# Performance work log

Measured on AMD Instinct MI355X. Metric: run time of the kernel, lower is better.

The kernel has to match this reference:

```python
import jax, jax.numpy as jnp
import numpy as np

E = 8      # num_experts
D = 1024   # input_size
H = 1024   # hidden_size
K = 2      # top_k
B = 2
S = 1024


def setup_inputs() -> dict:
    key = jax.random.key(0)
    ks = jax.random.split(key, 5)
    x = jax.random.normal(ks[0], (B, S, D), dtype=jnp.float32)
    p = jax.random.uniform(ks[1], (B * S, K), dtype=jnp.float32)
    expert_p = p / p.sum(axis=-1, keepdims=True)            # normalized top-k gates
    expert_idxs = jax.random.randint(ks[2], (B * S, K), 0, E)
    W1 = jax.random.normal(ks[3], (E, D, 2 * H), dtype=jnp.float32) * (D ** -0.5)
    W2 = jax.random.normal(ks[4], (E, H, D), dtype=jnp.float32) * (H ** -0.5)
    return {"x": x, "expert_p": expert_p, "expert_idxs": expert_idxs, "W1": W1, "W2": W2}


def reference(x, expert_p, expert_idxs, W1, W2):
    x_shape = x.shape
    xf = x.reshape(-1, x_shape[-1])                 # [N, D]
    n_tok = xf.shape[0]
    k = expert_idxs.shape[-1]
    x_pair = jnp.repeat(xf, k, axis=0)              # [N*K, D] token replicated per expert slot
    idx = expert_idxs.reshape(-1)                   # [N*K]
    p = expert_p.reshape(-1)                        # [N*K]
    y_pair = jnp.zeros((n_tok * k, x_shape[-1]), dtype=x.dtype)
    # loop over fixed small expert count; masked dense GEMM per expert
    for e in range(W1.shape[0]):
        m = (idx == e).astype(x.dtype)[:, None]     # [N*K, 1]
        hg = (x_pair * m) @ W1[e]                   # [N*K, 2H]
        h, g = jnp.split(hg, 2, axis=-1)            # chunk(2): (h, gates)
        a = jax.nn.silu(g) * h                      # SiLU-gated GLU
        y_pair = y_pair + (a @ W2[e]) * m           # [N*K, D]
    # combine: weight each pair by its gate prob and sum over top_k slots
    y = (y_pair * p[:, None]).reshape(n_tok, k, -1).sum(axis=1)
    return y.reshape(x_shape)
```

## Files before the change

### kernel.cpp

```cpp
#include <hip/hip_runtime.h>


typedef __bf16 bf16x8 __attribute__((ext_vector_type(8)));
typedef __bf16 bf16x4 __attribute__((ext_vector_type(4)));
typedef float  f32x4  __attribute__((ext_vector_type(4)));

#define NPAIR 4096
#define NTOK  2048
#define DDIM  1024
#define HDIM  1024
#define NEXP  8

#define ORDER_I   64
#define XB_OFF    (24576)
#define W1T_OFF   (XB_OFF + 4194304)
#define W2T_OFF   (W1T_OFF + 33554432)
#define ACT_OFF   (W2T_OFF + 16777216)

#define GLOAD_LDS16(g, l) \
    __builtin_amdgcn_global_load_lds( \
        (const __attribute__((address_space(1))) void*)(g), \
        (__attribute__((address_space(3))) void*)(l), 16, 0, 0)

__device__ __forceinline__ void tcvt_tile2(const float* __restrict__ s,
                                           __bf16* __restrict__ d,
                                           int R, int C, int k0, int c0,
                                           float (*tt)[65], int tid) {
#pragma unroll
    for (int p = 0; p < 8; p++) {
        int kr = p * 16 + (tid >> 4);
        int nc = (tid & 15) * 4;
        float4 v = *(const float4*)(s + (size_t)(k0 + kr) * C + c0 + nc);
        *(float4*)&tt[kr][nc] = v;
    }
    __syncthreads();
#pragma unroll
    for (int p = 0; p < 4; p++) {
        int cid = p * 256 + tid;
        int n = cid >> 4, kc = cid & 15;
        bf16x8 o;
#pragma unroll
        for (int j = 0; j < 8; j++) o[j] = (__bf16)tt[kc * 8 + j][n];
        *(bf16x8*)(d + (size_t)(c0 + n) * R + k0 + kc * 8) = o;
    }
}

__global__ __launch_bounds__(256) void prep_kernel(const float* __restrict__ x,
                                                   const float* __restrict__ W1,
                                                   const float* __restrict__ W2,
                                                   const int* __restrict__ idx,
                                                   int* __restrict__ wsi,
                                                   __bf16* __restrict__ xb,
                                                   __bf16* __restrict__ w1t,
                                                   __bf16* __restrict__ w2t,
                                                   float* __restrict__ out) {
    __shared__ float tt[128][65];
    __shared__ int cnt[NEXP];
    __shared__ int sbase, scur;
    const int b = blockIdx.x;
    const int tid = threadIdx.x;
    if (b < 2048) {
        int e = b >> 8, t2 = b & 255;
        int k0 = (t2 & 7) * 128, c0 = (t2 >> 3) * 64;
        tcvt_tile2(W1 + (size_t)e * DDIM * 2 * HDIM, w1t + (size_t)e * 2 * HDIM * DDIM,
                   DDIM, 2 * HDIM, k0, c0, tt, tid);
    } else if (b < 3072) {
        int b2 = b - 2048;
        int e = b2 >> 7, t2 = b2 & 127;
        int k0 = (t2 & 7) * 128, c0 = (t2 >> 3) * 64;
        tcvt_tile2(W2 + (size_t)e * HDIM * DDIM, w2t + (size_t)e * DDIM * HDIM,
                   HDIM, DDIM, k0, c0, tt, tid);
    } else if (b < 5120) {
        int i = (b - 3072) * 1024 + tid * 4;
        float4 v = *(const float4*)(x + i);
        bf16x4 o;
        o[0] = (__bf16)v.x; o[1] = (__bf16)v.y; o[2] = (__bf16)v.z; o[3] = (__bf16)v.w;
        *(bf16x4*)(xb + i) = o;
    } else if (b < 5632) {
        int base4 = (b - 5120) * 4096;
        float4 z = {0.f, 0.f, 0.f, 0.f};
#pragma unroll
        for (int j = 0; j < 4; j++)
            *(float4*)(out + base4 + j * 1024 + tid * 4) = z;
    } else {
        const int e = b - 5632;
        if (tid < NEXP) cnt[tid] = 0;
        if (tid == 0) scur = 0;
        __syncthreads();
        for (int i = tid; i < NPAIR; i += 256) atomicAdd(&cnt[idx[i] & 7], 1);
        __syncthreads();
        if (tid == 0) {
            int off = 0;
            for (int e2 = 0; e2 < NEXP; e2++) {
                if (e2 == e) { wsi[e] = cnt[e]; wsi[8 + e] = off; sbase = off; }
                off += (cnt[e2] + 127) & ~127;
            }
        }
        __syncthreads();
        for (int i = tid; i < NPAIR; i += 256) {
            if ((idx[i] & 7) == e) {
                int s = atomicAdd(&scur, 1);
                wsi[ORDER_I + sbase + s] = i;
            }
        }
    }
}

__global__ __launch_bounds__(256) void gemm1_kernel(const __bf16* __restrict__ xb,
                                                    const __bf16* __restrict__ w1t,
                                                    const int* __restrict__ wsi,
                                                    __bf16* __restrict__ act) {
    const int e = blockIdx.z;
    const int cnt = wsi[e];
    const int m0 = blockIdx.y * 128;
    if (m0 >= cnt) return;
    const int base = wsi[8 + e];
    const int n0 = blockIdx.x * 64;
    const int* order = wsi + ORDER_I;
    const __bf16* w1e = w1t + (size_t)e * 2048 * 1024;

    __shared__ __align__(16) __bf16 As[128][64];
    __shared__ __align__(16) __bf16 Bs[128][64];

    const int tid = threadIdx.x;
    const int lane = tid & 63, w = tid >> 6;
    const int lm = lane & 15, q = lane >> 4;
    const int wm = w & 1, wn = w >> 1;
    const int x7 = lm & 7;
    const int sw0 = (q ^ x7) * 16;
    const int sw1 = ((4 + q) ^ x7) * 16;

    const __bf16* ga[4];
    const __bf16* gb[4];
#pragma unroll
    for (int j = 0; j < 4; j++) {
        int c = j * 256 + tid;
        int r = c >> 3;
        int ks = ((c & 7) ^ (r & 7)) * 8;
        int m = m0 + r; if (m >= cnt) m = cnt - 1;
        int tok = order[base + m] >> 1;
        ga[j] = xb + (size_t)tok * DDIM + ks;
        int half = r >> 6, rr = r & 63;
        int rb = (rr < 32) ? (n0 + half * 32 + rr)
                           : (HDIM + n0 + half * 32 + (rr - 32));
        gb[j] = w1e + (size_t)rb * DDIM + ks;
    }

    f32x4 acc[4][4];
#pragma unroll
    for (int mt = 0; mt < 4; mt++)
#pragma unroll
        for (int nt = 0; nt < 4; nt++) acc[mt][nt] = (f32x4){0.f, 0.f, 0.f, 0.f};

    for (int k0 = 0; k0 < DDIM; k0 += 64) {
        __syncthreads();
#pragma unroll
        for (int j = 0; j < 4; j++) {
            int c = j * 256 + tid;
            GLOAD_LDS16(ga[j], (char*)&As[0][0] + c * 16);
            GLOAD_LDS16(gb[j], (char*)&Bs[0][0] + c * 16);
            ga[j] += 64; gb[j] += 64;
        }
        __syncthreads();
#pragma unroll
        for (int kh = 0; kh < 2; kh++) {
            const int sw = kh ? sw1 : sw0;
            bf16x8 af[4];
#pragma unroll
            for (int mt = 0; mt < 4; mt++)
                af[mt] = *(const bf16x8*)((const char*)&As[wm * 64 + mt * 16 + lm][0] + sw);
#pragma unroll
            for (int nt = 0; nt < 4; nt++) {
                bf16x8 bfr = *(const bf16x8*)((const char*)&Bs[wn * 64 + nt * 16 + lm][0] + sw);
#pragma unroll
                for (int mt = 0; mt < 4; mt++)
                    acc[mt][nt] = __builtin_amdgcn_mfma_f32_16x16x32_bf16(af[mt], bfr, acc[mt][nt], 0, 0, 0);
            }
        }
    }

#pragma unroll
    for (int mt = 0; mt < 4; mt++) {
        int mbase = m0 + wm * 64 + mt * 16 + q * 4;
#pragma unroll
        for (int ntp = 0; ntp < 2; ntp++) {
            int col = n0 + wn * 32 + ntp * 16 + lm;
#pragma unroll
            for (int r = 0; r < 4; r++) {
                int m = mbase + r;
                if (m < cnt) {
                    float h = acc[mt][ntp][r];
                    float g = acc[mt][ntp + 2][r];
                    float a = h * (g / (1.f + __expf(-g)));
                    act[(size_t)(base + m) * HDIM + col] = (__bf16)a;
                }
            }
        }
    }
}

__global__ __launch_bounds__(256) void gemm2_kernel(const __bf16* __restrict__ act,
                                                    const __bf16* __restrict__ w2t,
                                                    const int* __restrict__ wsi,
                                                    const float* __restrict__ p,
                                                    float* __restrict__ out) {
    const int e = blockIdx.z;
    const int cnt = wsi[e];
    const int m0 = blockIdx.y * 128;
    if (m0 >= cnt) return;
    const int base = wsi[8 + e];
    const int n0 = blockIdx.x * 64;
    const int* order = wsi + ORDER_I;
    const __bf16* w2e = w2t + (size_t)e * 1024 * 1024;

    __shared__ __align__(16) __bf16 As[128][64];
    __shared__ __align__(16) __bf16 Bs[64][64];

    const int tid = threadIdx.x;
    const int lane = tid & 63, w = tid >> 6;
    const int lm = lane & 15, q = lane >> 4;
    const int wm = w & 1, wn = w >> 1;
    const int x7 = lm & 7;
    const int sw0 = (q ^ x7) * 16;
    const int sw1 = ((4 + q) ^ x7) * 16;

    const __bf16* ga[4];
    const __bf16* gb[2];
#pragma unroll
    for (int j = 0; j < 4; j++) {
        int c = j * 256 + tid;
        int r = c >> 3;
        int ks = ((c & 7) ^ (r & 7)) * 8;
        ga[j] = act + (size_t)(base + m0 + r) * HDIM + ks;
    }
#pragma unroll
    for (int j = 0; j < 2; j++) {
        int c = j * 256 + tid;
        int r = c >> 3;
        int ks = ((c & 7) ^ (r & 7)) * 8;
        gb[j] = w2e + (size_t)(n0 + r) * HDIM + ks;
    }

    f32x4 acc[4][2];
#pragma unroll
    for (int mt = 0; mt < 4; mt++)
#pragma unroll
        for (int nt = 0; nt < 2; nt++) acc[mt][nt] = (f32x4){0.f, 0.f, 0.f, 0.f};

    for (int k0 = 0; k0 < HDIM; k0 += 64) {
        __syncthreads();
#pragma unroll
        for (int j = 0; j < 4; j++) {
            int c = j * 256 + tid;
            GLOAD_LDS16(ga[j], (char*)&As[0][0] + c * 16);
            ga[j] += 64;
        }
#pragma unroll
        for (int j = 0; j < 2; j++) {
            int c = j * 256 + tid;
            GLOAD_LDS16(gb[j], (char*)&Bs[0][0] + c * 16);
            gb[j] += 64;
        }
        __syncthreads();
#pragma unroll
        for (int kh = 0; kh < 2; kh++) {
            const int sw = kh ? sw1 : sw0;
            bf16x8 af[4];
#pragma unroll
            for (int mt = 0; mt < 4; mt++)
                af[mt] = *(const bf16x8*)((const char*)&As[wm * 64 + mt * 16 + lm][0] + sw);
#pragma unroll
            for (int nt = 0; nt < 2; nt++) {
                bf16x8 bfr = *(const bf16x8*)((const char*)&Bs[wn * 32 + nt * 16 + lm][0] + sw);
#pragma unroll
                for (int mt = 0; mt < 4; mt++)
                    acc[mt][nt] = __builtin_amdgcn_mfma_f32_16x16x32_bf16(af[mt], bfr, acc[mt][nt], 0, 0, 0);
            }
        }
    }

    int pi[4][4];
    float pw[4][4];
#pragma unroll
    for (int mt = 0; mt < 4; mt++)
#pragma unroll
        for (int r = 0; r < 4; r++) {
            int gm = m0 + wm * 64 + mt * 16 + q * 4 + r;
            if (gm < cnt) {
                int pr = order[base + gm];
                pi[mt][r] = pr;
                pw[mt][r] = p[pr];
            } else pi[mt][r] = -1;
        }
#pragma unroll
    for (int mt = 0; mt < 4; mt++)
#pragma unroll
        for (int nt = 0; nt < 2; nt++) {
            int col = n0 + wn * 32 + nt * 16 + lm;
#pragma unroll
            for (int r = 0; r < 4; r++) {
                if (pi[mt][r] >= 0) {
                    int tok = pi[mt][r] >> 1;
                    atomicAdd(out + (size_t)tok * DDIM + col, pw[mt][r] * acc[mt][nt][r]);
                }
            }
        }
}

extern "C" void kernel_launch(void* const* d_in, const int* in_sizes, int n_in,
                              void* d_out, int out_size, void* d_ws, size_t ws_size,
                              hipStream_t stream) {
    (void)in_sizes; (void)n_in; (void)out_size; (void)ws_size;
    const float* x   = (const float*)d_in[0];
    const float* p   = (const float*)d_in[1];
    const int* eidx  = (const int*)d_in[2];
    const float* W1  = (const float*)d_in[3];
    const float* W2  = (const float*)d_in[4];
    float* out = (float*)d_out;

    char* ws = (char*)d_ws;
    int* wsi     = (int*)ws;
    __bf16* xb   = (__bf16*)(ws + XB_OFF);
    __bf16* w1t  = (__bf16*)(ws + W1T_OFF);
    __bf16* w2t  = (__bf16*)(ws + W2T_OFF);
    __bf16* act  = (__bf16*)(ws + ACT_OFF);

    prep_kernel<<<5640, 256, 0, stream>>>(x, W1, W2, eidx, wsi, xb, w1t, w2t, out);
    gemm1_kernel<<<dim3(16, 32, NEXP), 256, 0, stream>>>(xb, w1t, wsi, act);
    gemm2_kernel<<<dim3(16, 32, NEXP), 256, 0, stream>>>(act, w2t, wsi, p, out);
}
```

Measured before the change: 221.8 us.

## Move W2 transpose and output zeroing into gemm1 launch to overlap

The W2 fp32-to-bf16 transpose and the output zero-fill move out of the prep kernel into extra z-slices of the gemm1 grid. This lets that memory-bound work run alongside the gemm1 tiles, many of which exit early for sparse experts. The transpose tile shrinks from 128x64 to 64x64, doubling the W1 block count in prep and cutting per-block LDS. gemm1's shared memory becomes one raw buffer that is reused as the transpose staging tile.

```diff
diff --git a/kernel.cpp b/kernel.cpp
--- a/kernel.cpp
+++ b/kernel.cpp
@@ -22,22 +22,21 @@
         (const __attribute__((address_space(1))) void*)(g), \
         (__attribute__((address_space(3))) void*)(l), 16, 0, 0)
 
-__device__ __forceinline__ void tcvt_tile2(const float* __restrict__ s,
-                                           __bf16* __restrict__ d,
-                                           int R, int C, int k0, int c0,
-                                           float (*tt)[65], int tid) {
-#pragma unroll
-    for (int p = 0; p < 8; p++) {
+__device__ __forceinline__ void tcvt64(const float* __restrict__ s,
+                                       __bf16* __restrict__ d,
+                                       int R, int C, int k0, int c0,
+                                       float (*tt)[65], int tid) {
+#pragma unroll
+    for (int p = 0; p < 4; p++) {
         int kr = p * 16 + (tid >> 4);
         int nc = (tid & 15) * 4;
-        float4 v = *(const float4*)(s + (size_t)(k0 + kr) * C + c0 + nc);
-        *(float4*)&tt[kr][nc] = v;
+        *(float4*)&tt[kr][nc] = *(const float4*)(s + (size_t)(k0 + kr) * C + c0 + nc);
     }
     __syncthreads();
 #pragma unroll
-    for (int p = 0; p < 4; p++) {
+    for (int p = 0; p < 2; p++) {
         int cid = p * 256 + tid;
-        int n = cid >> 4, kc = cid & 15;
+        int n = cid >> 3, kc = cid & 7;
         bf16x8 o;
 #pragma unroll
         for (int j = 0; j < 8; j++) o[j] = (__bf16)tt[kc * 8 + j][n];
@@ -47,43 +46,28 @@
 
 __global__ __launch_bounds__(256) void prep_kernel(const float* __restrict__ x,
                                                    const float* __restrict__ W1,
-                                                   const float* __restrict__ W2,
                                                    const int* __restrict__ idx,
                                                    int* __restrict__ wsi,
                                                    __bf16* __restrict__ xb,
-                                                   __bf16* __restrict__ w1t,
-                                                   __bf16* __restrict__ w2t,
-                                                   float* __restrict__ out) {
-    __shared__ float tt[128][65];
+                                                   __bf16* __restrict__ w1t) {
+    __shared__ float tt[64][65];
     __shared__ int cnt[NEXP];
     __shared__ int sbase, scur;
     const int b = blockIdx.x;
     const int tid = threadIdx.x;
-    if (b < 2048) {
-        int e = b >> 8, t2 = b & 255;
-        int k0 = (t2 & 7) * 128, c0 = (t2 >> 3) * 64;
-        tcvt_tile2(W1 + (size_t)e * DDIM * 2 * HDIM, w1t + (size_t)e * 2 * HDIM * DDIM,
-                   DDIM, 2 * HDIM, k0, c0, tt, tid);
-    } else if (b < 3072) {
-        int b2 = b - 2048;
-        int e = b2 >> 7, t2 = b2 & 127;
-        int k0 = (t2 & 7) * 128, c0 = (t2 >> 3) * 64;
-        tcvt_tile2(W2 + (size_t)e * HDIM * DDIM, w2t + (size_t)e * DDIM * HDIM,
-                   HDIM, DDIM, k0, c0, tt, tid);
-    } else if (b < 5120) {
-        int i = (b - 3072) * 1024 + tid * 4;
+    if (b < 4096) {
+        int e = b >> 9, t2 = b & 511;
+        int k0 = (t2 & 15) * 64, c0 = (t2 >> 4) * 64;
+        tcvt64(W1 + (size_t)e * DDIM * 2 * HDIM, w1t + (size_t)e * 2 * HDIM * DDIM,
+               DDIM, 2 * HDIM, k0, c0, tt, tid);
+    } else if (b < 6144) {
+        int i = (b - 4096) * 1024 + tid * 4;
         float4 v = *(const float4*)(x + i);
         bf16x4 o;
         o[0] = (__bf16)v.x; o[1] = (__bf16)v.y; o[2] = (__bf16)v.z; o[3] = (__bf16)v.w;
         *(bf16x4*)(xb + i) = o;
-    } else if (b < 5632) {
-        int base4 = (b - 5120) * 4096;
-        float4 z = {0.f, 0.f, 0.f, 0.f};
-#pragma unroll
-        for (int j = 0; j < 4; j++)
-            *(float4*)(out + base4 + j * 1024 + tid * 4) = z;
     } else {
-        const int e = b - 5632;
+        const int e = b - 6144;
         if (tid < NEXP) cnt[tid] = 0;
         if (tid == 0) scur = 0;
         __syncthreads();
@@ -109,8 +93,33 @@
 __global__ __launch_bounds__(256) void gemm1_kernel(const __bf16* __restrict__ xb,
                                                     const __bf16* __restrict__ w1t,
                                                     const int* __restrict__ wsi,
-                                                    __bf16* __restrict__ act) {
-    const int e = blockIdx.z;
+                                                    __bf16* __restrict__ act,
+                                                    const float* __restrict__ W2,
+                                                    __bf16* __restrict__ w2t,
+                                                    float* __restrict__ out) {
+    __shared__ __align__(16) char smem[32768];
+    const int tid = threadIdx.x;
+    const int z = blockIdx.z;
+
+    if (z >= 8) {
+        int aux = (z - 8) * 512 + blockIdx.y * 16 + blockIdx.x;
+        if (aux < 2048) {
+            int e = aux >> 8, t2 = aux & 255;
+            int k0 = (t2 & 15) * 64, c0 = (t2 >> 4) * 64;
+            tcvt64(W2 + (size_t)e * HDIM * DDIM, w2t + (size_t)e * DDIM * HDIM,
+                   HDIM, DDIM, k0, c0, (float (*)[65])smem, tid);
+        } else {
+            int zb = aux - 2048;
+            float4 z4 = {0.f, 0.f, 0.f, 0.f};
+            int b4 = zb * 4096;
+#pragma unroll
+            for (int j = 0; j < 4; j++)
+                *(float4*)(out + b4 + j * 1024 + tid * 4) = z4;
+        }
+        return;
+    }
+
+    const int e = z;
     const int cnt = wsi[e];
     const int m0 = blockIdx.y * 128;
     if (m0 >= cnt) return;
@@ -119,10 +128,9 @@
     const int* order = wsi + ORDER_I;
     const __bf16* w1e = w1t + (size_t)e * 2048 * 1024;
 
-    __shared__ __align__(16) __bf16 As[128][64];
-    __shared__ __align__(16) __bf16 Bs[128][64];
-
-    const int tid = threadIdx.x;
+    __bf16 (*As)[64] = (__bf16 (*)[64])smem;
+    __bf16 (*Bs)[64] = (__bf16 (*)[64])(smem + 16384);
+
     const int lane = tid & 63, w = tid >> 6;
     const int lm = lane & 15, q = lane >> 4;
     const int wm = w & 1, wn = w >> 1;
@@ -325,7 +333,7 @@
     __bf16* w2t  = (__bf16*)(ws + W2T_OFF);
     __bf16* act  = (__bf16*)(ws + ACT_OFF);
 
-    prep_kernel<<<5640, 256, 0, stream>>>(x, W1, W2, eidx, wsi, xb, w1t, w2t, out);
-    gemm1_kernel<<<dim3(16, 32, NEXP), 256, 0, stream>>>(xb, w1t, wsi, act);
+    prep_kernel<<<6152, 256, 0, stream>>>(x, W1, eidx, wsi, xb, w1t);
+    gemm1_kernel<<<dim3(16, 32, 13), 256, 0, stream>>>(xb, w1t, wsi, act, W2, w2t, out);
     gemm2_kernel<<<dim3(16, 32, NEXP), 256, 0, stream>>>(act, w2t, wsi, p, out);
 }
```

After: 216.6 us. 1.02x faster.
